# Kernel optimization log

Measured on AMD Instinct MI355X. Metric: run time of the kernel, lower is better.

## Reference

```python
import jax, jax.numpy as jnp
import numpy as np

HOP = 512
FAC = 4
FRAME_LEN = FAC * HOP  # 2048
ALPHA = 0.65
BETA = 0.06


def _inverse_stft_window():
    # torch.hann_window (periodic): w[n] = 0.5*(1 - cos(2*pi*n/N))
    n = np.arange(FRAME_LEN)
    w = 0.5 * (1.0 - np.cos(2.0 * np.pi * n / FRAME_LEN))
    denom = w ** 2
    # overlaps = ceil(frame_length / hop) == FAC (frame_length = FAC*HOP exactly)
    denom = denom.reshape(FAC, HOP).sum(axis=0)          # [HOP]
    denom = np.tile(denom, FAC)                          # [FRAME_LEN]
    return (w / denom).astype(np.float32)


def setup_inputs() -> dict:
    key = jax.random.key(0)
    B, F, T = 8, 1024, 2048
    stft_frames = jax.random.normal(key, (B, 2, F, T), dtype=jnp.float32)
    inv_window = jnp.asarray(_inverse_stft_window())
    return {"stft_frames": stft_frames, "inv_window": inv_window}


def reference(stft_frames, inv_window):
    # stft_frames: [B, 2, F, T] (real/imag stacked on dim 1)
    x = jnp.pad(stft_frames, ((0, 0), (0, 0), (0, 1), (0, 0)))  # F -> F+1 (Nyquist bin)
    real = x[:, 0] / BETA   # [B, F+1, T]
    imag = x[:, 1] / BETA
    # denormalize_complex: |x|^(1/alpha) * exp(i * atan2(im, re))
    mag = (real * real + imag * imag) ** (0.5 / ALPHA)
    theta = jnp.arctan2(imag, real)
    spec = jax.lax.complex(mag * jnp.cos(theta), mag * jnp.sin(theta))  # [B, F+1, T]
    frames = jnp.fft.irfft(spec, axis=-2)                 # [B, 2F, T], 2F == FRAME_LEN
    frames = jnp.transpose(frames, (0, 2, 1))             # [B, T, L]
    frames = frames * inv_window[None, None, :]
    B, T, L = frames.shape
    total = (T - 1) * HOP + L
    # vectorized overlap-add (scatter-add replacing the per-frame python loop)
    idx = (jnp.arange(T)[:, None] * HOP + jnp.arange(L)[None, :]).reshape(-1)  # [T*L]
    full = jnp.zeros((B, total), frames.dtype).at[:, idx].add(frames.reshape(B, -1))
    # output_buffer is empty on the first call; chunk = first hop*T samples
    return full[:, : HOP * T]
```

## Files before the change

### kernel.cpp

```cpp
#include <hip/hip_runtime.h>
#include <cstddef>


#define TDIM 2048
#define FDIM 1024
#define TT 8
#define NTOT (512 * 2048)
#define SSTR 20

static constexpr int kBREV[32] = {0,16,8,24,4,20,12,28,2,18,10,26,6,22,14,30,
                                  1,17,9,25,5,21,13,29,3,19,11,27,7,23,15,31};
static constexpr float kTR[16] = {
  1.0f, 0.98078528040323044f, 0.92387953251128674f, 0.83146961230254524f,
  0.70710678118654757f, 0.55557023301960218f, 0.38268343236508978f, 0.19509032201612825f,
  0.0f, -0.19509032201612825f, -0.38268343236508978f, -0.55557023301960218f,
  -0.70710678118654757f, -0.83146961230254524f, -0.92387953251128674f, -0.98078528040323044f};
static constexpr float kTI[16] = {
  0.0f, 0.19509032201612825f, 0.38268343236508978f, 0.55557023301960218f,
  0.70710678118654757f, 0.83146961230254524f, 0.92387953251128674f, 0.98078528040323044f,
  1.0f, 0.98078528040323044f, 0.92387953251128674f, 0.83146961230254524f,
  0.70710678118654757f, 0.55557023301960218f, 0.38268343236508978f, 0.19509032201612825f};

template <int H>
__device__ __forceinline__ void fft32_stage(float ar[32], float ai[32]) {
  constexpr int TSTEP = 16 / H;
  #pragma unroll
  for (int g = 0; g < 32; g += 2 * H) {
    #pragma unroll
    for (int j = 0; j < H; ++j) {
      const float twr = kTR[j * TSTEP];
      const float twi = kTI[j * TSTEP];
      const int i0 = g + j, i1 = i0 + H;
      const float tr = twr * ar[i1] - twi * ai[i1];
      const float ti = twr * ai[i1] + twi * ar[i1];
      ar[i1] = ar[i0] - tr; ai[i1] = ai[i0] - ti;
      ar[i0] += tr;         ai[i0] += ti;
    }
  }
}

__device__ __forceinline__ void ifft32_core(float ar[32], float ai[32]) {
  fft32_stage<1>(ar, ai);
  fft32_stage<2>(ar, ai);
  fft32_stage<4>(ar, ai);
  fft32_stage<8>(ar, ai);
  fft32_stage<16>(ar, ai);
}

__device__ __forceinline__ float pow_gain(float v, float PE, float KS) {
  return KS * __builtin_amdgcn_exp2f(PE * __builtin_amdgcn_logf(v));
}

__device__ __forceinline__ void denorm4(float4& r, float4& i, float PE, float KS) {
  float g;
  g = pow_gain(r.x * r.x + i.x * i.x, PE, KS); r.x *= g; i.x *= g;
  g = pow_gain(r.y * r.y + i.y * i.y, PE, KS); r.y *= g; i.y *= g;
  g = pow_gain(r.z * r.z + i.z * i.z, PE, KS); r.z *= g; i.z *= g;
  g = pow_gain(r.w * r.w + i.w * i.w, PE, KS); r.w *= g; i.w *= g;
}

template <int SC>
__device__ __forceinline__ int slot_row(int s) {
  return (SC == 0) ? (s < 256 ? s : s + 512) : (s + 256);
}

__device__ __forceinline__ void pack_pair_store(float* __restrict__ Sri,
    int sa, int sb, int cg, const float4& ar_, const float4& ai_,
    const float4& br_, const float4& bi_, int rowa) {
  const float ang = 3.0679615757712824e-3f * (float)rowa;
  const float ca = __cosf(ang), sn = __sinf(ang);
  const float arr[4] = {ar_.x, ar_.y, ar_.z, ar_.w};
  const float aii[4] = {ai_.x, ai_.y, ai_.z, ai_.w};
  const float brr[4] = {br_.x, br_.y, br_.z, br_.w};
  const float bii[4] = {bi_.x, bi_.y, bi_.z, bi_.w};
  float wa[8], wb[8];
  #pragma unroll
  for (int t = 0; t < 4; ++t) {
    const float Pre = arr[t] + brr[t], Pim = aii[t] - bii[t];
    const float Qre = arr[t] - brr[t], Qim = aii[t] + bii[t];
    const float u = ca * Qim + sn * Qre;
    const float v = ca * Qre - sn * Qim;
    wa[2*t] = Pre - u; wa[2*t+1] = Pim + v;
    wb[2*t] = Pre + u; wb[2*t+1] = v - Pim;
  }
  *(float4*)(Sri + sa * SSTR + 8 * cg)     = make_float4(wa[0], wa[1], wa[2], wa[3]);
  *(float4*)(Sri + sa * SSTR + 8 * cg + 4) = make_float4(wa[4], wa[5], wa[6], wa[7]);
  *(float4*)(Sri + sb * SSTR + 8 * cg)     = make_float4(wb[0], wb[1], wb[2], wb[3]);
  *(float4*)(Sri + sb * SSTR + 8 * cg + 4) = make_float4(wb[4], wb[5], wb[6], wb[7]);
}

__device__ __forceinline__ void dc_store(float* __restrict__ Sri, int cg,
                                         const float4& r) {
  *(float4*)(Sri + 8 * cg)     = make_float4(r.x, r.x, r.y, r.y);
  *(float4*)(Sri + 8 * cg + 4) = make_float4(r.z, r.z, r.w, r.w);
}

template <int SC>
__device__ __forceinline__ void stage1_read(const float* __restrict__ Sri,
                                            int q, int tl,
                                            float ar[32], float ai[32]) {
  #pragma unroll
  for (int u = 0; u < 16; ++u) {
    const int k2 = (SC == 0) ? (u < 8 ? u : u + 16) : (u + 8);
    const float2 w = *(const float2*)(Sri + (q + 32 * u) * SSTR + 2 * tl);
    ar[kBREV[k2]] = w.x; ai[kBREV[k2]] = w.y;
  }
}

#define XIDX(t, k1, r) ((k1) * 264 + (r) * 8 + (t))
#define FSTR 2054

__global__ __launch_bounds__(256) void istft_fused(const float* __restrict__ in,
                                                   const float* __restrict__ invw,
                                                   float* __restrict__ out) {
  __shared__ float buf[16896];
  float* Sri = buf;
  float* Xr  = buf;
  float* Xi  = buf + 8448;
  float* Fh  = buf;

  const int tid = threadIdx.x;
  const int tl  = tid & 7;
  const int q   = tid >> 3;

  const int id   = blockIdx.x;
  const int xcd  = id & 7;
  const int slot = id >> 3;
  const int b    = slot >> 5;
  const int tile = xcd * 32 + (slot & 31);
  const int t0   = tile * TT;

  const float* re_p = in + ((size_t)b * 2 + 0) * ((size_t)FDIM * TDIM);
  const float* im_p = in + ((size_t)b * 2 + 1) * ((size_t)FDIM * TDIM);

  const float KS = (float)(exp((-1.0 / 0.65) * log(0.06)) / 2048.0);
  const float PE = 7.0f / 26.0f;

  const int c  = tid >> 1;
  const int cg = tid & 1;
  int s_[4];
  if (c) { s_[0] = c; s_[1] = 512 - c; s_[2] = 128 + c; s_[3] = 384 - c; }
  else   { s_[0] = 0; s_[1] = 256;     s_[2] = 128;     s_[3] = 384;     }

  float ar[32], ai[32];

  {
    float4 reA[4], imA[4];
    #pragma unroll
    for (int j = 0; j < 4; ++j) {
      const int row = slot_row<0>(s_[j]);
      reA[j] = *(const float4*)(re_p + (size_t)row * TDIM + t0 + 4 * cg);
      imA[j] = *(const float4*)(im_p + (size_t)row * TDIM + t0 + 4 * cg);
    }
    float4 exR, exI;
    if (tid < 2) {
      exR = *(const float4*)(re_p + (size_t)256 * TDIM + t0 + 4 * tid);
      exI = *(const float4*)(im_p + (size_t)256 * TDIM + t0 + 4 * tid);
    }
    #pragma unroll
    for (int j = 0; j < 4; ++j) denorm4(reA[j], imA[j], PE, KS);
    if (tid < 2) denorm4(exR, exI, PE, KS);
    if (c) {
      pack_pair_store(Sri, s_[0], s_[1], cg, reA[0], imA[0], reA[1], imA[1], c);
      pack_pair_store(Sri, s_[2], s_[3], cg, reA[2], imA[2], reA[3], imA[3], 128 + c);
    } else {
      dc_store(Sri, cg, reA[0]);
      pack_pair_store(Sri, 128, 384, cg, reA[2], imA[2], reA[3], imA[3], 128);
      pack_pair_store(Sri, 256, 512, cg, reA[1], imA[1], exR, exI, 768);
    }

    float4 reB[4], imB[4];
    #pragma unroll
    for (int j = 0; j < 4; ++j) {
      const int row = slot_row<1>(s_[j]);
      reB[j] = *(const float4*)(re_p + (size_t)row * TDIM + t0 + 4 * cg);
      imB[j] = *(const float4*)(im_p + (size_t)row * TDIM + t0 + 4 * cg);
    }
    float4 exRB, exIB;
    if (tid < 2) {
      exRB = *(const float4*)(re_p + (size_t)768 * TDIM + t0 + 4 * tid);
      exIB = *(const float4*)(im_p + (size_t)768 * TDIM + t0 + 4 * tid);
    }
    __syncthreads();

    stage1_read<0>(Sri, q, tl, ar, ai);
    __syncthreads();

    #pragma unroll
    for (int j = 0; j < 4; ++j) denorm4(reB[j], imB[j], PE, KS);
    if (tid < 2) denorm4(exRB, exIB, PE, KS);
    if (c) {
      pack_pair_store(Sri, s_[0], s_[1], cg, reB[0], imB[0], reB[1], imB[1], 256 + c);
      pack_pair_store(Sri, s_[2], s_[3], cg, reB[2], imB[2], reB[3], imB[3], 384 + c);
    } else {
      pack_pair_store(Sri, 0, 512, cg, reB[0], imB[0], exRB, exIB, 256);
      pack_pair_store(Sri, 128, 384, cg, reB[2], imB[2], reB[3], imB[3], 384);
      pack_pair_store(Sri, 256, 256, cg, reB[1], imB[1], reB[1], imB[1], 512);
    }
    __syncthreads();
    stage1_read<1>(Sri, q, tl, ar, ai);
    __syncthreads();
  }

  ifft32_core(ar, ai);

  {
    const float aq2 = 6.1359231515425649e-3f * (float)q;
    const float dc = __cosf(aq2), dsn = __sinf(aq2);
    float cs = 1.0f, sn = 0.0f;
    #pragma unroll
    for (int r = 0; r < 32; ++r) {
      Xr[XIDX(tl, q, r)] = cs * ar[r] - sn * ai[r];
      Xi[XIDX(tl, q, r)] = cs * ai[r] + sn * ar[r];
      const float ncs = cs * dc - sn * dsn;
      sn = cs * dsn + sn * dc;
      cs = ncs;
    }
  }
  __syncthreads();
  float zr[32], zi[32];
  #pragma unroll
  for (int i = 0; i < 32; ++i) {
    zr[i] = Xr[XIDX(tl, kBREV[i], q)];
    zi[i] = Xi[XIDX(tl, kBREV[i], q)];
  }
  __syncthreads();

  ifft32_core(zr, zi);

  #pragma unroll
  for (int s = 0; s < 32; ++s) {
    const int l0 = 2 * q + 64 * s;
    const float2 w2 = *(const float2*)(invw + l0);
    float2 fv; fv.x = zr[s] * w2.x; fv.y = zi[s] * w2.y;
    *(float2*)(Fh + tl * FSTR + l0) = fv;
  }
  __syncthreads();

  float* ob = out + (size_t)b * NTOT;
  for (int rel = 0; rel < 11; ++rel) {
    const int tp = t0 + rel;
    if (tp > 2047) break;
    #pragma unroll
    for (int half = 0; half < 2; ++half) {
      const int j = tid + 256 * half;
      float v = 0.0f;
      #pragma unroll
      for (int cc = 0; cc < 4; ++cc) {
        const int tt = rel - cc;
        if (tt >= 0 && tt < TT) v += Fh[tt * FSTR + j + 512 * cc];
      }
      const int n = tp * 512 + j;
      if (rel >= 3 && rel <= 7) ob[n] = v;
      else atomicAdd(&ob[n], v);
    }
  }
}

extern "C" void kernel_launch(void* const* d_in, const int* in_sizes, int n_in,
                              void* d_out, int out_size, void* d_ws, size_t ws_size,
                              hipStream_t stream) {
  (void)in_sizes; (void)n_in; (void)d_ws; (void)ws_size;
  const float* in   = (const float*)d_in[0];
  const float* invw = (const float*)d_in[1];
  float* out = (float*)d_out;
  hipMemsetAsync(out, 0, (size_t)out_size * sizeof(float), stream);
  istft_fused<<<dim3(TDIM / TT * 8), 256, 0, stream>>>(in, invw, out);
}
```

Measured before the change: 228.9 us.

## Load all spectrum rows in one pass with rotated-store LDS layout

Replaces the two-phase load/pack/read of spectrum rows (half the rows per phase, two threads per row pair) with a single pass where each thread loads all 8 time columns for its four rows and packs 1024 rows into shared memory at once. The shared-memory row stride drops from 20 to 16 floats, and each thread rotates the order of its float4 stores to avoid bank conflicts. This removes two barriers and the serialized second load phase, exposing more memory-level parallelism. In exchange, more registers are live per thread and the packed buffer occupies more LDS at once.

Result: no change. 229.8 us (+0.4%).

```diff
diff --git a/kernel.cpp b/kernel.cpp
--- a/kernel.cpp
+++ b/kernel.cpp
@@ -6,7 +6,6 @@
 #define FDIM 1024
 #define TT 8
 #define NTOT (512 * 2048)
-#define SSTR 20
 
 static constexpr int kBREV[32] = {0,16,8,24,4,20,12,28,2,18,10,26,6,22,14,30,
                                   1,17,9,25,5,21,13,29,3,19,11,27,7,23,15,31};
@@ -59,52 +58,49 @@
   g = pow_gain(r.w * r.w + i.w * i.w, PE, KS); r.w *= g; i.w *= g;
 }
 
-template <int SC>
-__device__ __forceinline__ int slot_row(int s) {
-  return (SC == 0) ? (s < 256 ? s : s + 512) : (s + 256);
-}
-
-__device__ __forceinline__ void pack_pair_store(float* __restrict__ Sri,
-    int sa, int sb, int cg, const float4& ar_, const float4& ai_,
-    const float4& br_, const float4& bi_, int rowa) {
-  const float ang = 3.0679615757712824e-3f * (float)rowa;
+__device__ __forceinline__ void unpack8(const float4 v[2], float o[8]) {
+  o[0]=v[0].x; o[1]=v[0].y; o[2]=v[0].z; o[3]=v[0].w;
+  o[4]=v[1].x; o[5]=v[1].y; o[6]=v[1].z; o[7]=v[1].w;
+}
+
+__device__ __forceinline__ void store_row(float* __restrict__ S, int j,
+                                          const float w[16], int rot) {
+  #pragma unroll
+  for (int m = 0; m < 4; ++m) {
+    const int mm = (m + rot) & 3;
+    *(float4*)(S + j * 16 + 4 * mm) =
+        make_float4(w[4*mm], w[4*mm+1], w[4*mm+2], w[4*mm+3]);
+  }
+}
+
+__device__ __forceinline__ void pack_pair8(float* __restrict__ S, int ja, int jb,
+    const float4 ar4[2], const float4 ai4[2],
+    const float4 br4[2], const float4 bi4[2], int rot) {
+  float a_r[8], a_i[8], b_r[8], b_i[8];
+  unpack8(ar4, a_r); unpack8(ai4, a_i); unpack8(br4, b_r); unpack8(bi4, b_i);
+  const float ang = 3.0679615757712824e-3f * (float)ja;
   const float ca = __cosf(ang), sn = __sinf(ang);
-  const float arr[4] = {ar_.x, ar_.y, ar_.z, ar_.w};
-  const float aii[4] = {ai_.x, ai_.y, ai_.z, ai_.w};
-  const float brr[4] = {br_.x, br_.y, br_.z, br_.w};
-  const float bii[4] = {bi_.x, bi_.y, bi_.z, bi_.w};
-  float wa[8], wb[8];
-  #pragma unroll
-  for (int t = 0; t < 4; ++t) {
-    const float Pre = arr[t] + brr[t], Pim = aii[t] - bii[t];
-    const float Qre = arr[t] - brr[t], Qim = aii[t] + bii[t];
+  float wa[16], wb[16];
+  #pragma unroll
+  for (int t = 0; t < 8; ++t) {
+    const float Pre = a_r[t] + b_r[t], Pim = a_i[t] - b_i[t];
+    const float Qre = a_r[t] - b_r[t], Qim = a_i[t] + b_i[t];
     const float u = ca * Qim + sn * Qre;
     const float v = ca * Qre - sn * Qim;
-    wa[2*t] = Pre - u; wa[2*t+1] = Pim + v;
-    wb[2*t] = Pre + u; wb[2*t+1] = v - Pim;
-  }
-  *(float4*)(Sri + sa * SSTR + 8 * cg)     = make_float4(wa[0], wa[1], wa[2], wa[3]);
-  *(float4*)(Sri + sa * SSTR + 8 * cg + 4) = make_float4(wa[4], wa[5], wa[6], wa[7]);
-  *(float4*)(Sri + sb * SSTR + 8 * cg)     = make_float4(wb[0], wb[1], wb[2], wb[3]);
-  *(float4*)(Sri + sb * SSTR + 8 * cg + 4) = make_float4(wb[4], wb[5], wb[6], wb[7]);
-}
-
-__device__ __forceinline__ void dc_store(float* __restrict__ Sri, int cg,
-                                         const float4& r) {
-  *(float4*)(Sri + 8 * cg)     = make_float4(r.x, r.x, r.y, r.y);
-  *(float4*)(Sri + 8 * cg + 4) = make_float4(r.z, r.z, r.w, r.w);
-}
-
-template <int SC>
-__device__ __forceinline__ void stage1_read(const float* __restrict__ Sri,
-                                            int q, int tl,
-                                            float ar[32], float ai[32]) {
-  #pragma unroll
-  for (int u = 0; u < 16; ++u) {
-    const int k2 = (SC == 0) ? (u < 8 ? u : u + 16) : (u + 8);
-    const float2 w = *(const float2*)(Sri + (q + 32 * u) * SSTR + 2 * tl);
-    ar[kBREV[k2]] = w.x; ai[kBREV[k2]] = w.y;
-  }
+    wa[2*t] = Pre - u;  wa[2*t+1] = Pim + v;
+    wb[2*t] = Pre + u;  wb[2*t+1] = v - Pim;
+  }
+  store_row(S, ja, wa, rot);
+  store_row(S, jb, wb, rot);
+}
+
+__device__ __forceinline__ void dc8(float* __restrict__ S,
+                                    const float4 r4[2], int rot) {
+  float r[8]; unpack8(r4, r);
+  float w[16];
+  #pragma unroll
+  for (int t = 0; t < 8; ++t) { w[2*t] = r[t]; w[2*t+1] = r[t]; }
+  store_row(S, 0, w, rot);
 }
 
 #define XIDX(t, k1, r) ((k1) * 264 + (r) * 8 + (t))
@@ -136,73 +132,46 @@
   const float KS = (float)(exp((-1.0 / 0.65) * log(0.06)) / 2048.0);
   const float PE = 7.0f / 26.0f;
 
-  const int c  = tid >> 1;
-  const int cg = tid & 1;
-  int s_[4];
-  if (c) { s_[0] = c; s_[1] = 512 - c; s_[2] = 128 + c; s_[3] = 384 - c; }
-  else   { s_[0] = 0; s_[1] = 256;     s_[2] = 128;     s_[3] = 384;     }
+  {
+    int rows[4];
+    if (tid) { rows[0] = tid; rows[1] = 1024 - tid;
+               rows[2] = 256 + tid; rows[3] = 768 - tid; }
+    else     { rows[0] = 0; rows[1] = 512; rows[2] = 256; rows[3] = 768; }
+
+    float4 re[4][2], im[4][2];
+    #pragma unroll
+    for (int j = 0; j < 4; ++j) {
+      #pragma unroll
+      for (int h = 0; h < 2; ++h) {
+        re[j][h] = *(const float4*)(re_p + (size_t)rows[j] * TDIM + t0 + 4 * h);
+        im[j][h] = *(const float4*)(im_p + (size_t)rows[j] * TDIM + t0 + 4 * h);
+      }
+    }
+    #pragma unroll
+    for (int j = 0; j < 4; ++j) {
+      denorm4(re[j][0], im[j][0], PE, KS);
+      denorm4(re[j][1], im[j][1], PE, KS);
+    }
+    const int rot = (tid >> 1) & 3;
+    if (tid) {
+      pack_pair8(Sri, tid, 1024 - tid, re[0], im[0], re[1], im[1], rot);
+      pack_pair8(Sri, 256 + tid, 768 - tid, re[2], im[2], re[3], im[3], rot);
+    } else {
+      dc8(Sri, re[0], rot);
+      pack_pair8(Sri, 512, 512, re[1], im[1], re[1], im[1], rot);
+      pack_pair8(Sri, 256, 768, re[2], im[2], re[3], im[3], rot);
+    }
+  }
+  __syncthreads();
 
   float ar[32], ai[32];
-
-  {
-    float4 reA[4], imA[4];
-    #pragma unroll
-    for (int j = 0; j < 4; ++j) {
-      const int row = slot_row<0>(s_[j]);
-      reA[j] = *(const float4*)(re_p + (size_t)row * TDIM + t0 + 4 * cg);
-      imA[j] = *(const float4*)(im_p + (size_t)row * TDIM + t0 + 4 * cg);
-    }
-    float4 exR, exI;
-    if (tid < 2) {
-      exR = *(const float4*)(re_p + (size_t)256 * TDIM + t0 + 4 * tid);
-      exI = *(const float4*)(im_p + (size_t)256 * TDIM + t0 + 4 * tid);
-    }
-    #pragma unroll
-    for (int j = 0; j < 4; ++j) denorm4(reA[j], imA[j], PE, KS);
-    if (tid < 2) denorm4(exR, exI, PE, KS);
-    if (c) {
-      pack_pair_store(Sri, s_[0], s_[1], cg, reA[0], imA[0], reA[1], imA[1], c);
-      pack_pair_store(Sri, s_[2], s_[3], cg, reA[2], imA[2], reA[3], imA[3], 128 + c);
-    } else {
-      dc_store(Sri, cg, reA[0]);
-      pack_pair_store(Sri, 128, 384, cg, reA[2], imA[2], reA[3], imA[3], 128);
-      pack_pair_store(Sri, 256, 512, cg, reA[1], imA[1], exR, exI, 768);
-    }
-
-    float4 reB[4], imB[4];
-    #pragma unroll
-    for (int j = 0; j < 4; ++j) {
-      const int row = slot_row<1>(s_[j]);
-      reB[j] = *(const float4*)(re_p + (size_t)row * TDIM + t0 + 4 * cg);
-      imB[j] = *(const float4*)(im_p + (size_t)row * TDIM + t0 + 4 * cg);
-    }
-    float4 exRB, exIB;
-    if (tid < 2) {
-      exRB = *(const float4*)(re_p + (size_t)768 * TDIM + t0 + 4 * tid);
-      exIB = *(const float4*)(im_p + (size_t)768 * TDIM + t0 + 4 * tid);
-    }
-    __syncthreads();
-
-    stage1_read<0>(Sri, q, tl, ar, ai);
-    __syncthreads();
-
-    #pragma unroll
-    for (int j = 0; j < 4; ++j) denorm4(reB[j], imB[j], PE, KS);
-    if (tid < 2) denorm4(exRB, exIB, PE, KS);
-    if (c) {
-      pack_pair_store(Sri, s_[0], s_[1], cg, reB[0], imB[0], reB[1], imB[1], 256 + c);
-      pack_pair_store(Sri, s_[2], s_[3], cg, reB[2], imB[2], reB[3], imB[3], 384 + c);
-    } else {
-      pack_pair_store(Sri, 0, 512, cg, reB[0], imB[0], exRB, exIB, 256);
-      pack_pair_store(Sri, 128, 384, cg, reB[2], imB[2], reB[3], imB[3], 384);
-      pack_pair_store(Sri, 256, 256, cg, reB[1], imB[1], reB[1], imB[1], 512);
-    }
-    __syncthreads();
-    stage1_read<1>(Sri, q, tl, ar, ai);
-    __syncthreads();
-  }
-
+  #pragma unroll
+  for (int u = 0; u < 32; ++u) {
+    const float2 w = *(const float2*)(Sri + (q + 32 * u) * 16 + 2 * tl);
+    ar[kBREV[u]] = w.x; ai[kBREV[u]] = w.y;
+  }
   ifft32_core(ar, ai);
+  __syncthreads();
 
   {
     const float aq2 = 6.1359231515425649e-3f * (float)q;
```
